# Kernel tuning notes

Hardware: AMD Instinct MI355X
Metric: run time of the kernel (lower is better)

The kernel has to match this reference:

```python
import jax, jax.numpy as jnp
import numpy as np

N = 50000      # num nodes
E = 400000     # num edges
D = 384        # input_dim
H = 4          # heads
C = 128        # hidden_dim per head
HC = H * C     # 512


def setup_inputs() -> dict:
    key = jax.random.key(0)
    ks = jax.random.split(key, 32)
    w = lambda k, shape: jax.random.normal(k, shape, jnp.float32) * 0.05
    inp = {
        "x": jax.random.normal(ks[0], (N, D), jnp.float32),
        "edge_index": jax.random.randint(ks[1], (2, E), 0, N, dtype=jnp.int32),
    }
    dims = [(D, HC), (HC, HC)]  # layer0 in=384, layer1 in=512
    i = 2
    for l, (din, dout) in enumerate(dims):
        for nm in ["q", "k", "v", "s"]:  # query/key/value/skip linears
            inp[f"{nm}{l}_w"] = w(ks[i], (dout, din)); i += 1
            inp[f"{nm}{l}_b"] = jnp.zeros((dout,), jnp.float32)
    inp["out_w"] = w(ks[i], (D, HC))
    inp["out_b"] = jnp.zeros((D,), jnp.float32)
    return inp


def _transformer_conv(x, src, dst, Wq, bq, Wk, bk, Wv, bv, Ws, bs):
    # PyG TransformerConv, concat=True, root_weight=True, no edge features.
    n = x.shape[0]
    q = (x @ Wq.T + bq).reshape(n, H, C)
    k = (x @ Wk.T + bk).reshape(n, H, C)
    v = (x @ Wv.T + bv).reshape(n, H, C)
    # per-edge attention logits [E, H]; target = dst, source = src
    alpha = (q[dst] * k[src]).sum(-1) / jnp.sqrt(jnp.float32(C))
    m = jax.ops.segment_max(alpha, dst, num_segments=n)
    m = jnp.where(jnp.isfinite(m), m, 0.0)  # nodes with no in-edges
    e = jnp.exp(alpha - m[dst])
    denom = jax.ops.segment_sum(e, dst, num_segments=n)
    a = e / (denom[dst] + 1e-16)             # segment softmax [E, H]
    msg = v[src] * a[:, :, None]             # [E, H, C]
    agg = jax.ops.segment_sum(msg, dst, num_segments=n).reshape(n, HC)
    return agg + x @ Ws.T + bs               # + root/skip connection


def reference(x, edge_index,
              q0_w, q0_b, k0_w, k0_b, v0_w, v0_b, s0_w, s0_b,
              q1_w, q1_b, k1_w, k1_b, v1_w, v1_b, s1_w, s1_b,
              out_w, out_b):
    src, dst = edge_index[0], edge_index[1]
    h = _transformer_conv(x, src, dst, q0_w, q0_b, k0_w, k0_b, v0_w, v0_b, s0_w, s0_b)
    h = jax.nn.relu(h)
    h = _transformer_conv(h, src, dst, q1_w, q1_b, k1_w, k1_b, v1_w, v1_b, s1_w, s1_b)
    h = jax.nn.relu(h)
    return h @ out_w.T + out_b  # [N, D]
```

## Files before the change

### kernel.cpp

```cpp
#include <hip/hip_runtime.h>
#include <hip/hip_bf16.h>

#define NN 50000
#define NE 400000
#define DD 384
#define HC 512

typedef unsigned int u32;
typedef unsigned short u16;
typedef __attribute__((ext_vector_type(8))) short bf16x8;
typedef __attribute__((ext_vector_type(4))) float f32x4;

#define AS1 __attribute__((address_space(1)))
#define AS3 __attribute__((address_space(3)))

__device__ __forceinline__ float bflo(u32 u){ return __uint_as_float(u << 16); }
__device__ __forceinline__ float bfhi(u32 u){ return __uint_as_float(u & 0xFFFF0000u); }
__device__ __forceinline__ u16 f2bf(float f){
    u32 u = __float_as_uint(f);
    return (u16)((u + 0x7FFFu + ((u >> 16) & 1u)) >> 16);
}
__device__ __forceinline__ u32 pack2(float a, float b){
    return (u32)f2bf(a) | ((u32)f2bf(b) << 16);
}

template<int K>
__global__ __launch_bounds__(256)
void gemm_ws(const u16* __restrict__ Ab, const u16* __restrict__ Wb,
             const float* __restrict__ bias,
             u16* __restrict__ oQ, u16* __restrict__ oK,
             u16* __restrict__ oV, u16* __restrict__ oS)
{
    constexpr int NKT  = K / 64;
    constexpr int WCH  = K / 8;
    constexpr int NPAN = (NN + 127) / 128;
    __shared__ char smW[128 * K * 2];
    __shared__ char smA[2][16384];

    const int b   = blockIdx.x;
    const int xcd = b & 7;
    const int idx = b >> 3;
    const int ct  = idx & 15;
    const int rh  = idx >> 4;

    const int tid  = threadIdx.x;
    const int lane = tid & 63;
    const int w    = tid >> 6;
    const int wr   = w >> 1, wc = w & 1;
    const int r16  = lane & 15;
    const int kq   = lane >> 4;

    {
        const u16* W0 = Wb + (size_t)ct * 128 * K;
        #pragma unroll
        for (int p = 0; p < (128 * WCH) / 256; ++p) {
            int ci = p * 256 + tid;
            int row = ci / WCH, pc = ci % WCH;
            int lc = (pc & ~7) | ((pc ^ row) & 7);
            __builtin_amdgcn_global_load_lds((const AS1 u32*)(W0 + (size_t)row * K + lc * 8),
                                             (AS3 u32*)(smW + (size_t)ci * 16), 16, 0, 0);
        }
    }

    int np = 0;
    while ((2 * np + rh) * 8 + xcd < NPAN) ++np;
    const int total = np * NKT;

    auto stageA = [&](int t) {
        int jp = t / NKT, kc = t - jp * NKT;
        int m0 = ((2 * jp + rh) * 8 + xcd) * 128;
        #pragma unroll
        for (int p = 0; p < 4; ++p) {
            int ci = p * 256 + tid;
            int row = ci >> 3, pc = ci & 7;
            int lc = pc ^ (row & 7);
            int gr = m0 + row; if (gr >= NN) gr = NN - 1;
            __builtin_amdgcn_global_load_lds((const AS1 u32*)(Ab + (size_t)gr * K + kc * 64 + lc * 8),
                                             (AS3 u32*)(smA[t & 1] + ci * 16), 16, 0, 0);
        }
    };

    stageA(0);
    if (total > 1) stageA(1);

    f32x4 acc[4][4] = {};

    const int qsel = ct >> 2;
    u16* outp = (qsel == 0) ? oQ : (qsel == 1) ? oK : (qsel == 2) ? oV : oS;
    const int cb = (ct & 3) * 128 + wc * 64;
    float bb[4][4];
    #pragma unroll
    for (int ni = 0; ni < 4; ++ni)
        #pragma unroll
        for (int r = 0; r < 4; ++r)
            bb[ni][r] = bias[ct * 128 + wc * 64 + ni * 16 + kq * 4 + r];

    for (int t = 0; t < total; ++t) {
        const int jp = t / NKT, kc = t - jp * NKT;
        if (t + 1 >= total)                { asm volatile("s_waitcnt vmcnt(0)"  ::: "memory"); }
        else if (kc == 0 && t > 0)         { asm volatile("s_waitcnt vmcnt(20)" ::: "memory"); }
        else                               { asm volatile("s_waitcnt vmcnt(4)"  ::: "memory"); }
        __builtin_amdgcn_s_barrier();
        __builtin_amdgcn_sched_barrier(0);

        const char* pa = smA[t & 1] + (wr * 64) * 128;
        #pragma unroll
        for (int kk = 0; kk < 2; ++kk) {
            const int slot = (((kk << 2) + kq) ^ (r16 & 7)) << 4;
            bf16x8 av[4], bv[4];
            #pragma unroll
            for (int i = 0; i < 4; ++i) {
                av[i] = *(const bf16x8*)(pa + (i * 16 + r16) * 128 + slot);
                int rw = wc * 64 + i * 16 + r16;
                bv[i] = *(const bf16x8*)(smW + (size_t)rw * (K * 2) + kc * 128 + slot);
            }
            #pragma unroll
            for (int mi = 0; mi < 4; ++mi)
                #pragma unroll
                for (int ni = 0; ni < 4; ++ni)
                    acc[mi][ni] = __builtin_amdgcn_mfma_f32_16x16x32_bf16(
                        bv[ni], av[mi], acc[mi][ni], 0, 0, 0);
        }

        __builtin_amdgcn_sched_barrier(0);
        __builtin_amdgcn_s_barrier();
        __builtin_amdgcn_sched_barrier(0);

        if (kc == NKT - 1) {
            int m0 = ((2 * jp + rh) * 8 + xcd) * 128;
            #pragma unroll
            for (int mi = 0; mi < 4; ++mi) {
                int gr = m0 + wr * 64 + mi * 16 + r16;
                bool ok = gr < NN;
                #pragma unroll
                for (int ni = 0; ni < 4; ++ni) {
                    uint2 o;
                    o.x = pack2(acc[mi][ni][0] + bb[ni][0], acc[mi][ni][1] + bb[ni][1]);
                    o.y = pack2(acc[mi][ni][2] + bb[ni][2], acc[mi][ni][3] + bb[ni][3]);
                    if (ok) *(uint2*)(outp + (size_t)gr * 512 + cb + ni * 16 + kq * 4) = o;
                    #pragma unroll
                    for (int r = 0; r < 4; ++r) acc[mi][ni][r] = 0.f;
                }
            }
        }
        if (t + 2 < total) stageA(t + 2);
    }
}

template<int K>
__global__ __launch_bounds__(256)
void gemm2ph(const u16* __restrict__ Ab, const u16* __restrict__ Wb,
             const float* __restrict__ bias, float* __restrict__ oF,
             int n, int Ototal, int NT)
{
    constexpr int NKT = K / 64;
    __shared__ char smA[2][16384];
    __shared__ char smB[2][16384];

    const int nb  = gridDim.x;
    const int bd  = blockIdx.x;
    const int q8  = nb >> 3, r8 = nb & 7;
    const int xcd = bd & 7, gg = bd >> 3;
    const int tt  = (xcd < r8 ? xcd * (q8 + 1) : r8 * (q8 + 1) + (xcd - r8) * q8) + gg;
    const int m0  = (tt / NT) * 128;
    const int o0  = (tt % NT) * 128;

    const int tid  = threadIdx.x;
    const int lane = tid & 63;
    const int w    = tid >> 6;
    const int wr   = w >> 1, wc = w & 1;
    const int r16  = lane & 15;
    const int kq   = lane >> 4;

    auto stage = [&](int bf, int kt) {
        #pragma unroll
        for (int p = 0; p < 4; ++p) {
            int ci = p * 256 + tid, row = ci >> 3, pc = ci & 7;
            int lc = pc ^ (row & 7);
            const u16* g = Wb + (size_t)(o0 + row) * K + kt * 64 + lc * 8;
            __builtin_amdgcn_global_load_lds((const AS1 u32*)g,
                                             (AS3 u32*)(smB[bf] + ci * 16), 16, 0, 0);
        }
        #pragma unroll
        for (int p = 0; p < 4; ++p) {
            int ci = p * 256 + tid, row = ci >> 3, pc = ci & 7;
            int lc = pc ^ (row & 7);
            int gr = m0 + row; if (gr >= n) gr = n - 1;
            const u16* g = Ab + (size_t)gr * K + kt * 64 + lc * 8;
            __builtin_amdgcn_global_load_lds((const AS1 u32*)g,
                                             (AS3 u32*)(smA[bf] + ci * 16), 16, 0, 0);
        }
    };

    f32x4 acc[4][4] = {};

    stage(0, 0);
    stage(1, 1);

    for (int kt = 0; kt < NKT; ++kt) {
        if (kt + 1 < NKT) { asm volatile("s_waitcnt vmcnt(8)" ::: "memory"); }
        else             { asm volatile("s_waitcnt vmcnt(0)" ::: "memory"); }
        __builtin_amdgcn_s_barrier();
        __builtin_amdgcn_sched_barrier(0);

        const char* pa = smA[kt & 1] + (wr * 64) * 128;
        const char* pb = smB[kt & 1] + (wc * 64) * 128;
        #pragma unroll
        for (int kk = 0; kk < 2; ++kk) {
            const int slot = (((kk << 2) + kq) ^ (r16 & 7)) << 4;
            bf16x8 av[4], bv[4];
            #pragma unroll
            for (int i = 0; i < 4; ++i) {
                av[i] = *(const bf16x8*)(pa + (i * 16 + r16) * 128 + kk * 0 + slot + 0);
                bv[i] = *(const bf16x8*)(pb + (i * 16 + r16) * 128 + slot);
            }
            #pragma unroll
            for (int mi = 0; mi < 4; ++mi)
                #pragma unroll
                for (int ni = 0; ni < 4; ++ni)
                    acc[mi][ni] = __builtin_amdgcn_mfma_f32_16x16x32_bf16(
                        bv[ni], av[mi], acc[mi][ni], 0, 0, 0);
        }

        __builtin_amdgcn_sched_barrier(0);
        __builtin_amdgcn_s_barrier();
        __builtin_amdgcn_sched_barrier(0);
        if (kt + 2 < NKT) stage(kt & 1, kt + 2);
    }

    #pragma unroll
    for (int mi = 0; mi < 4; ++mi) {
        int gr = m0 + wr * 64 + mi * 16 + r16;
        if (gr >= n) continue;
        #pragma unroll
        for (int ni = 0; ni < 4; ++ni) {
            int col = o0 + wc * 64 + ni * 16 + kq * 4;
            float4 o = make_float4(acc[mi][ni][0] + bias[col],
                                   acc[mi][ni][1] + bias[col + 1],
                                   acc[mi][ni][2] + bias[col + 2],
                                   acc[mi][ni][3] + bias[col + 3]);
            *(float4*)(oF + (size_t)gr * Ototal + col) = o;
        }
    }
}

#define XG  2400000
#define W0G 24576
#define W1G 32768
#define WOG 24576
#define CVT_TOTAL (XG + 4*W0G + 4*W1G + WOG)

__global__ __launch_bounds__(256)
void cvt_all(const float* __restrict__ x,
             const float* q0w, const float* k0w, const float* v0w, const float* s0w,
             const float* q1w, const float* k1w, const float* v1w, const float* s1w,
             const float* ow,
             u16* __restrict__ Xb, u16* __restrict__ Wc0,
             u16* __restrict__ Wc1, u16* __restrict__ WcO)
{
    int i = blockIdx.x * 256 + threadIdx.x;
    if (i >= CVT_TOTAL) return;
    const float* s; u16* d; int g;
    if (i < XG) { s = x; d = Xb; g = i; }
    else {
        int j = i - XG;
        if (j < 4 * W0G) {
            int q = j / W0G; g = j - q * W0G;
            s = (q == 0 ? q0w : q == 1 ? k0w : q == 2 ? v0w : s0w);
            d = Wc0 + (size_t)q * W0G * 8;
        } else if ((j -= 4 * W0G) < 4 * W1G) {
            int q = j / W1G; g = j - q * W1G;
            s = (q == 0 ? q1w : q == 1 ? k1w : q == 2 ? v1w : s1w);
            d = Wc1 + (size_t)q * W1G * 8;
        } else { j -= 4 * W1G; s = ow; d = WcO; g = j; }
    }
    float4 f0 = ((const float4*)s)[(size_t)g * 2];
    float4 f1 = ((const float4*)s)[(size_t)g * 2 + 1];
    uint4 o;
    o.x = pack2(f0.x, f0.y); o.y = pack2(f0.z, f0.w);
    o.z = pack2(f1.x, f1.y); o.w = pack2(f1.z, f1.w);
    ((uint4*)d)[g] = o;
}

__global__ __launch_bounds__(256)
void pack_bias(const float* q0, const float* k0, const float* v0, const float* s0,
               const float* q1, const float* k1, const float* v1, const float* s1,
               const float* ob, float* __restrict__ dst)
{
    int i = blockIdx.x * 256 + threadIdx.x;
    if (i >= 4480) return;
    float v;
    if (i < 2048) {
        int j = i & 511, q = i >> 9;
        v = (q == 0 ? q0 : q == 1 ? k0 : q == 2 ? v0 : s0)[j];
    } else if (i < 4096) {
        int j = i - 2048; int q = j >> 9; j &= 511;
        v = (q == 0 ? q1 : q == 1 ? k1 : q == 2 ? v1 : s1)[j];
    } else {
        v = ob[i - 4096];
    }
    dst[i] = v;
}

__global__ __launch_bounds__(256)
void zero_deg(int* __restrict__ deg)
{
    int i = blockIdx.x * 256 + threadIdx.x;
    if (i < NN) deg[i] = 0;
}

__global__ __launch_bounds__(256)
void hist_dst(const int* __restrict__ dst, int* __restrict__ deg)
{
    int e = blockIdx.x * 256 + threadIdx.x;
    if (e < NE) atomicAdd(&deg[dst[e]], 1);
}

__global__ __launch_bounds__(1024)
void scan_deg(const int* __restrict__ deg, int* __restrict__ rowptr,
              int* __restrict__ cursor)
{
    __shared__ int wsum[16];
    const int tid = threadIdx.x, lane = tid & 63, wid = tid >> 6;
    int carry = 0;
    for (int base = 0; base < NN; base += 1024) {
        int i = base + tid;
        int orig = (i < NN) ? deg[i] : 0;
        int v = orig;
        #pragma unroll
        for (int off = 1; off < 64; off <<= 1) {
            int t = __shfl_up(v, off, 64);
            if (lane >= off) v += t;
        }
        if (lane == 63) wsum[wid] = v;
        __syncthreads();
        if (wid == 0) {
            int s = (lane < 16) ? wsum[lane] : 0;
            #pragma unroll
            for (int off = 1; off < 16; off <<= 1) {
                int t = __shfl_up(s, off, 16);
                if ((lane & 15) >= off) s += t;
            }
            if (lane < 16) wsum[lane] = s;
        }
        __syncthreads();
        int woff  = (wid == 0) ? 0 : wsum[wid - 1];
        int total = wsum[15];
        int excl  = carry + woff + (v - orig);
        if (i < NN) { rowptr[i] = excl; cursor[i] = excl; }
        carry += total;
        __syncthreads();
    }
    if (tid == 0) rowptr[NN] = NE;
}

__global__ __launch_bounds__(256)
void scatter_edges(const int* __restrict__ src, const int* __restrict__ dst,
                   int* __restrict__ cursor, int* __restrict__ esrc_ord)
{
    int e = blockIdx.x * 256 + threadIdx.x;
    if (e >= NE) return;
    int pos = atomicAdd(&cursor[dst[e]], 1);
    esrc_ord[pos] = src[e];
}

__global__ __launch_bounds__(256)
void node_attn(const u16* __restrict__ Qb, const u16* __restrict__ Kb,
               const u16* __restrict__ Vb, const int* __restrict__ rowptr,
               const int* __restrict__ esrc, const u16* __restrict__ skipb,
               u16* __restrict__ outb)
{
    int d = blockIdx.x * 4 + (threadIdx.x >> 6);
    if (d >= NN) return;
    int lane = threadIdx.x & 63;

    uint4 qv = *((const uint4*)(Qb + (size_t)d * HC) + lane);
    float q[8] = { bflo(qv.x), bfhi(qv.x), bflo(qv.y), bfhi(qv.y),
                   bflo(qv.z), bfhi(qv.z), bflo(qv.w), bfhi(qv.w) };

    int beg = rowptr[d], end = rowptr[d + 1];
    float m = -INFINITY, den = 0.f;
    float acc[8] = {};

    for (int i = beg; i < end; ++i) {
        int s = esrc[i];
        uint4 kv = *((const uint4*)(Kb + (size_t)s * HC) + lane);
        float sum = q[0] * bflo(kv.x) + q[1] * bfhi(kv.x)
                  + q[2] * bflo(kv.y) + q[3] * bfhi(kv.y)
                  + q[4] * bflo(kv.z) + q[5] * bfhi(kv.z)
                  + q[6] * bflo(kv.w) + q[7] * bfhi(kv.w);
        #pragma unroll
        for (int off = 1; off < 16; off <<= 1) sum += __shfl_xor(sum, off, 64);
        float alpha = sum * 0.08838834764831845f;

        float mnew  = fmaxf(m, alpha);
        float scale = __expf(m - mnew);
        float p     = __expf(alpha - mnew);
        den = den * scale + p;

        uint4 vv = *((const uint4*)(Vb + (size_t)s * HC) + lane);
        acc[0] = acc[0] * scale + p * bflo(vv.x);
        acc[1] = acc[1] * scale + p * bfhi(vv.x);
        acc[2] = acc[2] * scale + p * bflo(vv.y);
        acc[3] = acc[3] * scale + p * bfhi(vv.y);
        acc[4] = acc[4] * scale + p * bflo(vv.z);
        acc[5] = acc[5] * scale + p * bfhi(vv.z);
        acc[6] = acc[6] * scale + p * bflo(vv.w);
        acc[7] = acc[7] * scale + p * bfhi(vv.w);
        m = mnew;
    }

    float inv = 1.f / (den + 1e-16f);
    size_t base = (size_t)d * HC + lane * 8;
    uint4 sv = *((const uint4*)(skipb + base));
    float sk[8] = { bflo(sv.x), bfhi(sv.x), bflo(sv.y), bfhi(sv.y),
                    bflo(sv.z), bfhi(sv.z), bflo(sv.w), bfhi(sv.w) };
    uint4 o;
    o.x = pack2(fmaxf(acc[0] * inv + sk[0], 0.f), fmaxf(acc[1] * inv + sk[1], 0.f));
    o.y = pack2(fmaxf(acc[2] * inv + sk[2], 0.f), fmaxf(acc[3] * inv + sk[3], 0.f));
    o.z = pack2(fmaxf(acc[4] * inv + sk[4], 0.f), fmaxf(acc[5] * inv + sk[5], 0.f));
    o.w = pack2(fmaxf(acc[6] * inv + sk[6], 0.f), fmaxf(acc[7] * inv + sk[7], 0.f));
    *(uint4*)(outb + base) = o;
}

extern "C" void kernel_launch(void* const* d_in, const int* in_sizes, int n_in,
                              void* d_out, int out_size, void* d_ws, size_t ws_size,
                              hipStream_t stream)
{
    const float* x   = (const float*)d_in[0];
    const int* ei    = (const int*)d_in[1];
    const int* esrc  = ei;
    const int* edst  = ei + NE;
    const float* q0w = (const float*)d_in[2];  const float* q0b = (const float*)d_in[3];
    const float* k0w = (const float*)d_in[4];  const float* k0b = (const float*)d_in[5];
    const float* v0w = (const float*)d_in[6];  const float* v0b = (const float*)d_in[7];
    const float* s0w = (const float*)d_in[8];  const float* s0b = (const float*)d_in[9];
    const float* q1w = (const float*)d_in[10]; const float* q1b = (const float*)d_in[11];
    const float* k1w = (const float*)d_in[12]; const float* k1b = (const float*)d_in[13];
    const float* v1w = (const float*)d_in[14]; const float* v1b = (const float*)d_in[15];
    const float* s1w = (const float*)d_in[16]; const float* s1b = (const float*)d_in[17];
    const float* ow  = (const float*)d_in[18]; const float* obs = (const float*)d_in[19];

    char* p = (char*)d_ws;
    auto take = [&](size_t bytes) { void* r = (void*)p; p += (bytes + 255) & ~(size_t)255; return r; };
    u16*   Qb     = (u16*)take((size_t)NN * HC * 2);
    u16*   Vb     = (u16*)take((size_t)NN * HC * 2);
    u16*   Hb     = (u16*)take((size_t)NN * HC * 2);
    u16*   Sb     = (u16*)take((size_t)NN * HC * 2);
    u16*   Xb     = (u16*)take((size_t)NN * DD * 2);
    u16*   Wc0    = (u16*)take((size_t)2048 * DD * 2);
    u16*   Wc1    = (u16*)take((size_t)2048 * HC * 2);
    u16*   WcO    = (u16*)take((size_t)DD * HC * 2);
    float* barena = (float*)take(4480 * 4);

    char* dob = (char*)d_out;
    u16* Kb       = (u16*)dob;
    int* deg      = (int*)(dob + 51200000);
    int* rowptr   = (int*)(dob + 51400192);
    int* cursor   = (int*)(dob + 51600384);
    int* esrc_ord = (int*)(dob + 51800576);

    dim3 blk(256);
    int gN   = (NN + 255) / 256;
    int gE   = (NE + 255) / 256;
    int gnod = (NN + 3) / 4;
    const int NPAN = (NN + 127) / 128;
    int go = NPAN * 3;

    pack_bias<<<(4480 + 255) / 256, blk, 0, stream>>>(q0b, k0b, v0b, s0b,
                                                      q1b, k1b, v1b, s1b, obs, barena);
    cvt_all<<<(CVT_TOTAL + 255) / 256, blk, 0, stream>>>(x,
        q0w, k0w, v0w, s0w, q1w, k1w, v1w, s1w, ow, Xb, Wc0, Wc1, WcO);

    zero_deg      <<<gN, blk, 0, stream>>>(deg);
    hist_dst      <<<gE, blk, 0, stream>>>(edst, deg);
    scan_deg      <<<1, 1024, 0, stream>>>(deg, rowptr, cursor);
    scatter_edges <<<gE, blk, 0, stream>>>(esrc, edst, cursor, esrc_ord);

    gemm_ws<DD><<<256, 256, 0, stream>>>(Xb, Wc0, barena, Qb, Kb, Vb, Sb);
    node_attn<<<gnod, blk, 0, stream>>>(Qb, Kb, Vb, rowptr, esrc_ord, Sb, Hb);

    gemm_ws<HC><<<256, 256, 0, stream>>>(Hb, Wc1, barena + 2048, Qb, Kb, Vb, Sb);
    node_attn<<<gnod, blk, 0, stream>>>(Qb, Kb, Vb, rowptr, esrc_ord, Sb, Hb);

    gemm2ph<HC><<<go, blk, 0, stream>>>(Hb, WcO, barena + 4096,
                                        (float*)d_out, NN, 384, 3);
}
```

Before: 811.9 us.

## Use 8-wave blocks in persistent QKVS GEMM and prefetch next edge in attention

The weight-stationary QKVS GEMM now launches 512 threads per block, with each of 8 waves computing a 32x64 sub-tile instead of 64x64. Staging loops and vmcnt thresholds are rescaled to match. The goal is more waves per CU to hide LDS and global latency, at the cost of more LDS reads of the W tile per MFMA. Separately, node_attn software-prefetches the next edge's K and V rows while it computes the current one, to overlap gather latency with the online-softmax math at the cost of extra registers.

```diff
diff --git a/kernel.cpp b/kernel.cpp
--- a/kernel.cpp
+++ b/kernel.cpp
@@ -25,7 +25,7 @@
 }
 
 template<int K>
-__global__ __launch_bounds__(256)
+__global__ __launch_bounds__(512)
 void gemm_ws(const u16* __restrict__ Ab, const u16* __restrict__ Wb,
              const float* __restrict__ bias,
              u16* __restrict__ oQ, u16* __restrict__ oK,
@@ -46,15 +46,16 @@
     const int tid  = threadIdx.x;
     const int lane = tid & 63;
     const int w    = tid >> 6;
-    const int wr   = w >> 1, wc = w & 1;
+    const int wq   = w >> 1;
+    const int wc   = w & 1;
     const int r16  = lane & 15;
     const int kq   = lane >> 4;
 
     {
         const u16* W0 = Wb + (size_t)ct * 128 * K;
         #pragma unroll
-        for (int p = 0; p < (128 * WCH) / 256; ++p) {
-            int ci = p * 256 + tid;
+        for (int p = 0; p < (128 * WCH) / 512; ++p) {
+            int ci = p * 512 + tid;
             int row = ci / WCH, pc = ci % WCH;
             int lc = (pc & ~7) | ((pc ^ row) & 7);
             __builtin_amdgcn_global_load_lds((const AS1 u32*)(W0 + (size_t)row * K + lc * 8),
@@ -70,8 +71,8 @@
         int jp = t / NKT, kc = t - jp * NKT;
         int m0 = ((2 * jp + rh) * 8 + xcd) * 128;
         #pragma unroll
-        for (int p = 0; p < 4; ++p) {
-            int ci = p * 256 + tid;
+        for (int p = 0; p < 2; ++p) {
+            int ci = p * 512 + tid;
             int row = ci >> 3, pc = ci & 7;
             int lc = pc ^ (row & 7);
             int gr = m0 + row; if (gr >= NN) gr = NN - 1;
@@ -83,7 +84,7 @@
     stageA(0);
     if (total > 1) stageA(1);
 
-    f32x4 acc[4][4] = {};
+    f32x4 acc[2][4] = {};
 
     const int qsel = ct >> 2;
     u16* outp = (qsel == 0) ? oQ : (qsel == 1) ? oK : (qsel == 2) ? oV : oS;
@@ -97,25 +98,27 @@
 
     for (int t = 0; t < total; ++t) {
         const int jp = t / NKT, kc = t - jp * NKT;
-        if (t + 1 >= total)                { asm volatile("s_waitcnt vmcnt(0)"  ::: "memory"); }
-        else if (kc == 0 && t > 0)         { asm volatile("s_waitcnt vmcnt(20)" ::: "memory"); }
-        else                               { asm volatile("s_waitcnt vmcnt(4)"  ::: "memory"); }
+        if (t + 1 >= total)        { asm volatile("s_waitcnt vmcnt(0)"  ::: "memory"); }
+        else if (kc == 0 && t > 0) { asm volatile("s_waitcnt vmcnt(10)" ::: "memory"); }
+        else                       { asm volatile("s_waitcnt vmcnt(2)"  ::: "memory"); }
         __builtin_amdgcn_s_barrier();
         __builtin_amdgcn_sched_barrier(0);
 
-        const char* pa = smA[t & 1] + (wr * 64) * 128;
+        const char* bufA = smA[t & 1];
         #pragma unroll
         for (int kk = 0; kk < 2; ++kk) {
             const int slot = (((kk << 2) + kq) ^ (r16 & 7)) << 4;
-            bf16x8 av[4], bv[4];
+            bf16x8 av[2], bv[4];
+            #pragma unroll
+            for (int i = 0; i < 2; ++i)
+                av[i] = *(const bf16x8*)(bufA + (wq * 32 + i * 16 + r16) * 128 + slot);
             #pragma unroll
             for (int i = 0; i < 4; ++i) {
-                av[i] = *(const bf16x8*)(pa + (i * 16 + r16) * 128 + slot);
                 int rw = wc * 64 + i * 16 + r16;
                 bv[i] = *(const bf16x8*)(smW + (size_t)rw * (K * 2) + kc * 128 + slot);
             }
             #pragma unroll
-            for (int mi = 0; mi < 4; ++mi)
+            for (int mi = 0; mi < 2; ++mi)
                 #pragma unroll
                 for (int ni = 0; ni < 4; ++ni)
                     acc[mi][ni] = __builtin_amdgcn_mfma_f32_16x16x32_bf16(
@@ -129,8 +132,8 @@
         if (kc == NKT - 1) {
             int m0 = ((2 * jp + rh) * 8 + xcd) * 128;
             #pragma unroll
-            for (int mi = 0; mi < 4; ++mi) {
-                int gr = m0 + wr * 64 + mi * 16 + r16;
+            for (int mi = 0; mi < 2; ++mi) {
+                int gr = m0 + wq * 32 + mi * 16 + r16;
                 bool ok = gr < NN;
                 #pragma unroll
                 for (int ni = 0; ni < 4; ++ni) {
@@ -211,7 +214,7 @@
             bf16x8 av[4], bv[4];
             #pragma unroll
             for (int i = 0; i < 4; ++i) {
-                av[i] = *(const bf16x8*)(pa + (i * 16 + r16) * 128 + kk * 0 + slot + 0);
+                av[i] = *(const bf16x8*)(pa + (i * 16 + r16) * 128 + slot);
                 bv[i] = *(const bf16x8*)(pb + (i * 16 + r16) * 128 + slot);
             }
             #pragma unroll
@@ -382,32 +385,41 @@
     float m = -INFINITY, den = 0.f;
     float acc[8] = {};
 
-    for (int i = beg; i < end; ++i) {
-        int s = esrc[i];
-        uint4 kv = *((const uint4*)(Kb + (size_t)s * HC) + lane);
-        float sum = q[0] * bflo(kv.x) + q[1] * bfhi(kv.x)
-                  + q[2] * bflo(kv.y) + q[3] * bfhi(kv.y)
-                  + q[4] * bflo(kv.z) + q[5] * bfhi(kv.z)
-                  + q[6] * bflo(kv.w) + q[7] * bfhi(kv.w);
-        #pragma unroll
-        for (int off = 1; off < 16; off <<= 1) sum += __shfl_xor(sum, off, 64);
-        float alpha = sum * 0.08838834764831845f;
-
-        float mnew  = fmaxf(m, alpha);
-        float scale = __expf(m - mnew);
-        float p     = __expf(alpha - mnew);
-        den = den * scale + p;
-
-        uint4 vv = *((const uint4*)(Vb + (size_t)s * HC) + lane);
-        acc[0] = acc[0] * scale + p * bflo(vv.x);
-        acc[1] = acc[1] * scale + p * bfhi(vv.x);
-        acc[2] = acc[2] * scale + p * bflo(vv.y);
-        acc[3] = acc[3] * scale + p * bfhi(vv.y);
-        acc[4] = acc[4] * scale + p * bflo(vv.z);
-        acc[5] = acc[5] * scale + p * bfhi(vv.z);
-        acc[6] = acc[6] * scale + p * bflo(vv.w);
-        acc[7] = acc[7] * scale + p * bfhi(vv.w);
-        m = mnew;
+    if (beg < end) {
+        int s0 = esrc[beg];
+        uint4 kv = *((const uint4*)(Kb + (size_t)s0 * HC) + lane);
+        uint4 vv = *((const uint4*)(Vb + (size_t)s0 * HC) + lane);
+
+        for (int i = beg; i < end; ++i) {
+            uint4 kc = kv, vc = vv;
+            if (i + 1 < end) {
+                int sn = esrc[i + 1];
+                kv = *((const uint4*)(Kb + (size_t)sn * HC) + lane);
+                vv = *((const uint4*)(Vb + (size_t)sn * HC) + lane);
+            }
+            float sum = q[0] * bflo(kc.x) + q[1] * bfhi(kc.x)
+                      + q[2] * bflo(kc.y) + q[3] * bfhi(kc.y)
+                      + q[4] * bflo(kc.z) + q[5] * bfhi(kc.z)
+                      + q[6] * bflo(kc.w) + q[7] * bfhi(kc.w);
+            #pragma unroll
+            for (int off = 1; off < 16; off <<= 1) sum += __shfl_xor(sum, off, 64);
+            float alpha = sum * 0.08838834764831845f;
+
+            float mnew  = fmaxf(m, alpha);
+            float scale = __expf(m - mnew);
+            float p     = __expf(alpha - mnew);
+            den = den * scale + p;
+
+            acc[0] = acc[0] * scale + p * bflo(vc.x);
+            acc[1] = acc[1] * scale + p * bfhi(vc.x);
+            acc[2] = acc[2] * scale + p * bflo(vc.y);
+            acc[3] = acc[3] * scale + p * bfhi(vc.y);
+            acc[4] = acc[4] * scale + p * bflo(vc.z);
+            acc[5] = acc[5] * scale + p * bfhi(vc.z);
+            acc[6] = acc[6] * scale + p * bflo(vc.w);
+            acc[7] = acc[7] * scale + p * bfhi(vc.w);
+            m = mnew;
+        }
     }
 
     float inv = 1.f / (den + 1e-16f);
@@ -477,10 +489,10 @@
     scan_deg      <<<1, 1024, 0, stream>>>(deg, rowptr, cursor);
     scatter_edges <<<gE, blk, 0, stream>>>(esrc, edst, cursor, esrc_ord);
 
-    gemm_ws<DD><<<256, 256, 0, stream>>>(Xb, Wc0, barena, Qb, Kb, Vb, Sb);
+    gemm_ws<DD><<<256, 512, 0, stream>>>(Xb, Wc0, barena, Qb, Kb, Vb, Sb);
     node_attn<<<gnod, blk, 0, stream>>>(Qb, Kb, Vb, rowptr, esrc_ord, Sb, Hb);
 
-    gemm_ws<HC><<<256, 256, 0, stream>>>(Hb, Wc1, barena + 2048, Qb, Kb, Vb, Sb);
+    gemm_ws<HC><<<256, 512, 0, stream>>>(Hb, Wc1, barena + 2048, Qb, Kb, Vb, Sb);
     node_attn<<<gnod, blk, 0, stream>>>(Qb, Kb, Vb, rowptr, esrc_ord, Sb, Hb);
 
     gemm2ph<HC><<<go, blk, 0, stream>>>(Hb, WcO, barena + 4096,
```

Result: faster. 792.3 us (-2.4%).
